# Optimization experiments

Measured on AMD Instinct MI355X. Metric: run time of the kernel, lower is better.

Reference implementation:

```python
import jax, jax.numpy as jnp
import numpy as np

B, T, C = 2, 1024, 2048
H, N = 32, 64
D_DECAY, D_A, D_G = 64, 64, 128
FFN = 8192


def setup_inputs() -> dict:
    key = jax.random.key(0)
    ks = iter(jax.random.split(key, 40))
    def nrm(shape, s):
        return jax.random.normal(next(ks), shape, jnp.float32) * s
    return {
        "x": nrm((B, T, C), 1.0),
        "x_prev": nrm((B, C), 1.0),
        "state": jnp.zeros((B, H, N, N), jnp.float32),
        "ln1_w": jnp.ones((C,), jnp.float32),
        "ln2_w": jnp.ones((C,), jnp.float32),
        "x_r": nrm((C,), 0.1), "x_w": nrm((C,), 0.1), "x_k": nrm((C,), 0.1),
        "x_v": nrm((C,), 0.1), "x_a": nrm((C,), 0.1), "x_g": nrm((C,), 0.1),
        "w0": nrm((C,), 0.1), "w1": nrm((C, D_DECAY), 0.02), "w2": nrm((D_DECAY, C), 0.02),
        "a0": nrm((C,), 0.1), "a1": nrm((C, D_A), 0.02), "a2": nrm((D_A, C), 0.02),
        "g1": nrm((C, D_G), 0.02), "g2": nrm((D_G, C), 0.02),
        "k_k": nrm((C,), 0.1), "k_a": nrm((C,), 0.1), "r_k": nrm((C,), 0.1),
        "R_": nrm((C, C), 0.02), "K_": nrm((C, C), 0.02),
        "V_": nrm((C, C), 0.02), "O_": nrm((C, C), 0.02),
        "gate_w": nrm((FFN, C), 0.02), "up_w": nrm((FFN, C), 0.02),
        "down_w": nrm((C, FFN), 0.02),
    }


def _rmsnorm(h, w, eps=1e-6):
    hf = h.astype(jnp.float32)
    var = jnp.mean(hf * hf, axis=-1, keepdims=True)
    return (w * (hf * jax.lax.rsqrt(var + eps))).astype(h.dtype)


def _lin(x, W):  # nn.Linear weight layout [out, in]
    return jnp.einsum('btc,oc->bto', x, W)


def _rwkv7_scan(r, logw, k, v, a, b, s0):
    # r/logw/k/v/a/b: [B,T,H,N]; s0: [B,H,N,N] (rows=value dim, cols=key dim)
    decay = jnp.exp(logw)  # logw = -exp(w_pre) < 0, per Step2
    def step(S, ins):
        rt, dt, kt, vt, at, bt = ins  # each [B,H,N]
        sa = jnp.einsum('bhvk,bhk->bhv', S, at)
        S = S * dt[:, :, None, :] + sa[..., None] * bt[:, :, None, :] + vt[..., None] * kt[:, :, None, :]
        o = jnp.einsum('bhvk,bhk->bhv', S, rt)
        return S, o
    xs = tuple(jnp.swapaxes(t, 0, 1) for t in (r, decay, k, v, a, b))  # -> [T,B,H,N]
    S, out = jax.lax.scan(step, s0, xs)
    return jnp.swapaxes(out, 0, 1), S  # [B,T,H,N], [B,H,N,N]


def reference(x, x_prev, state, ln1_w, ln2_w, x_r, x_w, x_k, x_v, x_a, x_g,
              w0, w1, w2, a0, a1, a2, g1, g2, k_k, k_a, r_k,
              R_, K_, V_, O_, gate_w, up_w, down_w):
    # ---- ln1 + token shift (Step1), layer_id == 0 so v_first = v ----
    xn = _rmsnorm(x, ln1_w)
    sx = jnp.concatenate([x_prev[:, None, :], xn[:, :-1]], axis=1) - xn
    xr = xn + sx * x_r; xw = xn + sx * x_w; xk = xn + sx * x_k
    xv = xn + sx * x_v; xa = xn + sx * x_a; xg = xn + sx * x_g
    r = _lin(xr, R_)
    w_pre = -jax.nn.softplus(-(w0 + jnp.tanh(xw @ w1) @ w2)) - 0.5
    k = _lin(xk, K_)
    v = _lin(xv, V_)
    a = jax.nn.sigmoid(a0 + (xa @ a1) @ a2)
    g = jax.nn.sigmoid(xg @ g1) @ g2
    kk = (k * k_k).reshape(B, T, H, N)
    kk = kk / jnp.maximum(jnp.linalg.norm(kk, axis=-1, keepdims=True), 1e-12)
    kk = kk.reshape(B, T, C)
    k = k * (1.0 + (a - 1.0) * k_a)
    aa = -kk
    bb = kk * a
    # ---- Step2: RWKV-7 recurrent scan ----
    logw = -jnp.exp(w_pre)
    shp = (B, T, H, N)
    out, new_state = _rwkv7_scan(r.reshape(shp), logw.reshape(shp), k.reshape(shp),
                                 v.reshape(shp), aa.reshape(shp), bb.reshape(shp), state)
    # ---- Step3: bonus term, gate, output proj ----
    xx = out.reshape(B, T, C)
    bonus = ((r * k * r_k).reshape(shp).sum(-1, keepdims=True) * v.reshape(shp)).reshape(B, T, C)
    att = _lin((xx + bonus) * g, O_)
    x = x + att
    # ---- ln2 + SwiGLU MLP ----
    xn2 = _rmsnorm(x, ln2_w)
    mlp = _lin(jax.nn.silu(_lin(xn2, gate_w)) * _lin(xn2, up_w), down_w)
    return x + mlp
```

## Files before the change

kernel.cpp:

```cpp
#include <hip/hip_runtime.h>
#include <hip/hip_bf16.h>
#include <stdint.h>


#define B_   2
#define T_   1024
#define C_   2048
#define H_   32
#define BT_  (B_*T_)
#define FFN_ 8192

typedef unsigned short u16;
typedef __bf16 bf16x8 __attribute__((ext_vector_type(8)));
typedef u16 ushx8 __attribute__((ext_vector_type(8)));
typedef float floatx4 __attribute__((ext_vector_type(4)));

__device__ __forceinline__ float bf2f(u16 v) {
    unsigned int u = ((unsigned int)v) << 16;
    return __builtin_bit_cast(float, u);
}
__device__ __forceinline__ u16 f2bf(float f) {
    unsigned int u = __builtin_bit_cast(unsigned int, f);
    unsigned int lsb = (u >> 16) & 1u;
    u += 0x7fffu + lsb;
    return (u16)(u >> 16);
}

__global__ __launch_bounds__(256) void rmsnorm_kernel(
    const float* __restrict__ in, const float* __restrict__ wgt,
    float* __restrict__ outf, u16* __restrict__ outb, int bf)
{
    int row = blockIdx.x;
    int tid = threadIdx.x;
    const float* xp = in + (size_t)row * C_;
    int c = tid * 8;
    float4 v0 = *(const float4*)&xp[c];
    float4 v1 = *(const float4*)&xp[c + 4];
    float ss = v0.x*v0.x + v0.y*v0.y + v0.z*v0.z + v0.w*v0.w
             + v1.x*v1.x + v1.y*v1.y + v1.z*v1.z + v1.w*v1.w;
    #pragma unroll
    for (int m = 1; m < 64; m <<= 1) ss += __shfl_xor(ss, m, 64);
    __shared__ float red[4];
    if ((tid & 63) == 0) red[tid >> 6] = ss;
    __syncthreads();
    ss = red[0] + red[1] + red[2] + red[3];
    float scale = 1.0f / sqrtf(ss / (float)C_ + 1e-6f);
    float vals[8] = {v0.x, v0.y, v0.z, v0.w, v1.x, v1.y, v1.z, v1.w};
    size_t base = (size_t)row * C_ + c;
    if (bf) {
        #pragma unroll
        for (int j = 0; j < 8; j++) outb[base + j] = f2bf(wgt[c + j] * vals[j] * scale);
    } else {
        #pragma unroll
        for (int j = 0; j < 8; j++) outf[base + j] = wgt[c + j] * vals[j] * scale;
    }
}

__global__ __launch_bounds__(256) void mix_kernel(
    const float* __restrict__ xn, const float* __restrict__ x_prev,
    const float* __restrict__ mr, const float* __restrict__ mw,
    const float* __restrict__ mk, const float* __restrict__ mv,
    const float* __restrict__ ma, const float* __restrict__ mg,
    u16* __restrict__ oxr, u16* __restrict__ oxw, u16* __restrict__ oxk,
    u16* __restrict__ oxv, u16* __restrict__ oxa, u16* __restrict__ oxg)
{
    int row = blockIdx.x;
    int b = row / T_;
    int t = row - b * T_;
    int c = threadIdx.x * 8;
    size_t base = (size_t)row * C_ + c;
    const float* prev = (t == 0) ? (x_prev + (size_t)b * C_ + c) : (xn + base - C_);
    #pragma unroll
    for (int j = 0; j < 8; j++) {
        float xc = xn[base + j];
        float sx = prev[j] - xc;
        int cc = c + j;
        oxr[base + j] = f2bf(xc + sx * mr[cc]);
        oxw[base + j] = f2bf(xc + sx * mw[cc]);
        oxk[base + j] = f2bf(xc + sx * mk[cc]);
        oxv[base + j] = f2bf(xc + sx * mv[cc]);
        oxa[base + j] = f2bf(xc + sx * ma[cc]);
        oxg[base + j] = f2bf(xc + sx * mg[cc]);
    }
}

__global__ __launch_bounds__(256) void cvt_bf16_kernel(
    const float* __restrict__ in, u16* __restrict__ out, long n)
{
    long i = ((long)blockIdx.x * 256 + threadIdx.x) * 4;
    if (i + 3 >= n) return;
    float4 v = *(const float4*)&in[i];
    out[i]     = f2bf(v.x);
    out[i + 1] = f2bf(v.y);
    out[i + 2] = f2bf(v.z);
    out[i + 3] = f2bf(v.w);
}

__global__ __launch_bounds__(256) void transpose_kernel(
    const float* __restrict__ in, u16* __restrict__ out, int rows_in, int cols_in)
{
    long idx = (long)blockIdx.x * 256 + threadIdx.x;
    long total = (long)rows_in * cols_in;
    if (idx >= total) return;
    long o = idx / rows_in;
    long i = idx - o * rows_in;
    out[idx] = f2bf(in[i * (long)cols_in + o]);
}

#define LSTR 40
template<int BN>
__global__ __launch_bounds__(256, 2) void gemm_kernel(
    const u16* __restrict__ A, const u16* __restrict__ W,
    float* __restrict__ Cf, u16* __restrict__ Cb,
    const float* __restrict__ Of, const u16* __restrict__ Ob,
    int M, int N, int K, int mode)
{
    constexpr int IN = BN / 32;
    __shared__ u16 As[128 * LSTR];
    __shared__ u16 Ws[BN * LSTR];
    const int tid = threadIdx.x;
    const int bm = blockIdx.y, bn = blockIdx.x;
    const int row0 = bm * 128, col0 = bn * BN;
    const int wave = tid >> 6, lane = tid & 63;
    const int wr = wave >> 1, wc = wave & 1;
    const int q = lane >> 4, l16 = lane & 15;

    floatx4 acc[4][IN];
    #pragma unroll
    for (int i = 0; i < 4; i++)
        #pragma unroll
        for (int j = 0; j < IN; j++) acc[i][j] = (floatx4){0.f, 0.f, 0.f, 0.f};

    const int r0 = tid >> 2;
    const int cb0 = (tid & 3) * 8;

    for (int k0 = 0; k0 < K; k0 += 32) {
        __syncthreads();
        {
            ushx8 va0 = *(const ushx8*)&A[(size_t)(row0 + r0) * K + k0 + cb0];
            ushx8 vw0 = *(const ushx8*)&W[(size_t)(col0 + r0) * K + k0 + cb0];
            ushx8 va1 = *(const ushx8*)&A[(size_t)(row0 + r0 + 64) * K + k0 + cb0];
            *(ushx8*)&As[r0 * LSTR + cb0] = va0;
            *(ushx8*)&Ws[r0 * LSTR + cb0] = vw0;
            *(ushx8*)&As[(r0 + 64) * LSTR + cb0] = va1;
            if (BN == 128) {
                ushx8 vw1 = *(const ushx8*)&W[(size_t)(col0 + r0 + 64) * K + k0 + cb0];
                *(ushx8*)&Ws[(r0 + 64) * LSTR + cb0] = vw1;
            }
        }
        __syncthreads();
        bf16x8 af[4], wf[IN];
        #pragma unroll
        for (int im = 0; im < 4; im++) {
            int r = wr * 64 + im * 16 + l16;
            af[im] = __builtin_bit_cast(bf16x8, *(const ushx8*)&As[r * LSTR + q * 8]);
        }
        #pragma unroll
        for (int in_ = 0; in_ < IN; in_++) {
            int r = wc * (BN / 2) + in_ * 16 + l16;
            wf[in_] = __builtin_bit_cast(bf16x8, *(const ushx8*)&Ws[r * LSTR + q * 8]);
        }
        #pragma unroll
        for (int im = 0; im < 4; im++)
            #pragma unroll
            for (int in_ = 0; in_ < IN; in_++)
                acc[im][in_] = __builtin_amdgcn_mfma_f32_16x16x32_bf16(
                    af[im], wf[in_], acc[im][in_], 0, 0, 0);
    }

    #pragma unroll
    for (int im = 0; im < 4; im++) {
        #pragma unroll
        for (int in_ = 0; in_ < IN; in_++) {
            #pragma unroll
            for (int rg = 0; rg < 4; rg++) {
                int row = row0 + wr * 64 + im * 16 + q * 4 + rg;
                int col = col0 + wc * (BN / 2) + in_ * 16 + l16;
                if (row < M && col < N) {
                    size_t idx = (size_t)row * N + col;
                    float v = acc[im][in_][rg];
                    switch (mode) {
                        case 0: Cf[idx] = v; break;
                        case 1: Cb[idx] = f2bf(v * bf2f(Ob[idx])); break;
                        case 2: { float s = v / (1.f + expf(-v)); Cb[idx] = f2bf(s); } break;
                        case 3: Cf[idx] = v + Of[idx]; break;
                        case 4: Cb[idx] = f2bf(tanhf(v)); break;
                        case 5: Cb[idx] = f2bf(1.f / (1.f + expf(-v))); break;
                        case 6: Cb[idx] = f2bf(v); break;
                    }
                }
            }
        }
    }
}

__global__ __launch_bounds__(256) void decay_kernel(
    float* __restrict__ z, const float* __restrict__ w0)
{
    long i = (long)blockIdx.x * 256 + threadIdx.x;
    int c = (int)(i & (C_ - 1));
    float zp = w0[c] + z[i];
    float xneg = -zp;
    float sp = (xneg > 20.f) ? xneg : log1pf(expf(xneg));
    float wpre = -sp - 0.5f;
    z[i] = expf(-expf(wpre));
}

__global__ __launch_bounds__(256) void siga_kernel(
    float* __restrict__ z, const float* __restrict__ a0)
{
    long i = (long)blockIdx.x * 256 + threadIdx.x;
    int c = (int)(i & (C_ - 1));
    z[i] = 1.f / (1.f + expf(-(a0[c] + z[i])));
}

__global__ __launch_bounds__(256) void kknorm_kernel(
    float* __restrict__ k, const float* __restrict__ a,
    const float* __restrict__ k_k, const float* __restrict__ k_a,
    float* __restrict__ kk)
{
    int row = blockIdx.x;
    int c = threadIdx.x * 8;
    size_t base = (size_t)row * C_ + c;
    float kl[8], kkl[8];
    float ss = 0.f;
    #pragma unroll
    for (int j = 0; j < 8; j++) {
        kl[j] = k[base + j];
        float t = kl[j] * k_k[c + j];
        kkl[j] = t;
        ss += t * t;
    }
    ss += __shfl_xor(ss, 1, 64);
    ss += __shfl_xor(ss, 2, 64);
    ss += __shfl_xor(ss, 4, 64);
    float inv = 1.f / fmaxf(sqrtf(ss), 1e-12f);
    #pragma unroll
    for (int j = 0; j < 8; j++) {
        kk[base + j] = kkl[j] * inv;
        float av = a[base + j];
        k[base + j] = kl[j] * (1.f + (av - 1.f) * k_a[c + j]);
    }
}

#define SB 16
__global__ __launch_bounds__(256) void scan_kernel(
    const float* __restrict__ rp, const float* __restrict__ dp,
    const float* __restrict__ kp, const float* __restrict__ kkp,
    const float* __restrict__ ap, const float* __restrict__ vp,
    const float* __restrict__ st0, float* __restrict__ xx)
{
    int blk = blockIdx.x;
    int bh = blk >> 2, vblk = blk & 3;
    int b = bh >> 5, h = bh & 31;
    int tid = threadIdx.x;
    int vloc = tid >> 4, kg = tid & 15, c0 = kg * 4;
    int vrow = vblk * 16 + vloc;
    float S0, S1, S2, S3;
    {
        const float* sp = st0 + ((size_t)bh * 64 + vrow) * 64 + c0;
        S0 = sp[0]; S1 = sp[1]; S2 = sp[2]; S3 = sp[3];
    }
    __shared__ float Rs[SB][64], Ds[SB][64], Ks[SB][64], KKs[SB][64], As[SB][64], Vs[SB][64];
    int sidx = (tid * 4) >> 6;
    int nidx = (tid * 4) & 63;
    for (int t0 = 0; t0 < T_; t0 += SB) {
        __syncthreads();
        size_t g = ((size_t)b * T_ + t0 + sidx) * C_ + h * 64 + nidx;
        *(float4*)&Rs[sidx][nidx]  = *(const float4*)&rp[g];
        *(float4*)&Ds[sidx][nidx]  = *(const float4*)&dp[g];
        *(float4*)&Ks[sidx][nidx]  = *(const float4*)&kp[g];
        *(float4*)&KKs[sidx][nidx] = *(const float4*)&kkp[g];
        *(float4*)&As[sidx][nidx]  = *(const float4*)&ap[g];
        *(float4*)&Vs[sidx][nidx]  = *(const float4*)&vp[g];
        __syncthreads();
        for (int s = 0; s < SB; s++) {
            float4 dv  = *(const float4*)&Ds[s][c0];
            float4 kv  = *(const float4*)&Ks[s][c0];
            float4 kkv = *(const float4*)&KKs[s][c0];
            float4 av  = *(const float4*)&As[s][c0];
            float4 rv  = *(const float4*)&Rs[s][c0];
            float vt = Vs[s][vrow];
            float sa = -(S0 * kkv.x + S1 * kkv.y + S2 * kkv.z + S3 * kkv.w);
            sa += __shfl_xor(sa, 1, 64);
            sa += __shfl_xor(sa, 2, 64);
            sa += __shfl_xor(sa, 4, 64);
            sa += __shfl_xor(sa, 8, 64);
            S0 = S0 * dv.x + sa * (kkv.x * av.x) + vt * kv.x;
            S1 = S1 * dv.y + sa * (kkv.y * av.y) + vt * kv.y;
            S2 = S2 * dv.z + sa * (kkv.z * av.z) + vt * kv.z;
            S3 = S3 * dv.w + sa * (kkv.w * av.w) + vt * kv.w;
            float o = S0 * rv.x + S1 * rv.y + S2 * rv.z + S3 * rv.w;
            o += __shfl_xor(o, 1, 64);
            o += __shfl_xor(o, 2, 64);
            o += __shfl_xor(o, 4, 64);
            o += __shfl_xor(o, 8, 64);
            if (kg == 0)
                xx[((size_t)b * T_ + t0 + s) * C_ + h * 64 + vrow] = o;
        }
    }
}

__global__ __launch_bounds__(256) void ygate_kernel(
    const float* __restrict__ xx, const float* __restrict__ r,
    const float* __restrict__ k, const float* __restrict__ r_k,
    const float* __restrict__ v, const float* __restrict__ g,
    u16* __restrict__ y)
{
    int row = blockIdx.x;
    int c = threadIdx.x * 8;
    size_t base = (size_t)row * C_ + c;
    float bsum = 0.f;
    #pragma unroll
    for (int j = 0; j < 8; j++) bsum += r[base + j] * k[base + j] * r_k[c + j];
    bsum += __shfl_xor(bsum, 1, 64);
    bsum += __shfl_xor(bsum, 2, 64);
    bsum += __shfl_xor(bsum, 4, 64);
    #pragma unroll
    for (int j = 0; j < 8; j++) {
        float yv = (xx[base + j] + bsum * v[base + j]) * g[base + j];
        y[base + j] = f2bf(yv);
    }
}

extern "C" void kernel_launch(void* const* d_in, const int* in_sizes, int n_in,
                              void* d_out, int out_size, void* d_ws, size_t ws_size,
                              hipStream_t stream)
{
    const float* x      = (const float*)d_in[0];
    const float* x_prev = (const float*)d_in[1];
    const float* state  = (const float*)d_in[2];
    const float* ln1_w  = (const float*)d_in[3];
    const float* ln2_w  = (const float*)d_in[4];
    const float* x_r = (const float*)d_in[5];
    const float* x_w = (const float*)d_in[6];
    const float* x_k = (const float*)d_in[7];
    const float* x_v = (const float*)d_in[8];
    const float* x_a = (const float*)d_in[9];
    const float* x_g = (const float*)d_in[10];
    const float* w0 = (const float*)d_in[11];
    const float* w1 = (const float*)d_in[12];
    const float* w2 = (const float*)d_in[13];
    const float* a0 = (const float*)d_in[14];
    const float* a1 = (const float*)d_in[15];
    const float* a2 = (const float*)d_in[16];
    const float* g1 = (const float*)d_in[17];
    const float* g2 = (const float*)d_in[18];
    const float* k_k = (const float*)d_in[19];
    const float* k_a = (const float*)d_in[20];
    const float* r_k = (const float*)d_in[21];
    const float* Rw = (const float*)d_in[22];
    const float* Kw = (const float*)d_in[23];
    const float* Vw = (const float*)d_in[24];
    const float* Ow = (const float*)d_in[25];
    const float* gate_w = (const float*)d_in[26];
    const float* up_w   = (const float*)d_in[27];
    const float* down_w = (const float*)d_in[28];
    float* out = (float*)d_out;

    const size_t MBc = 1024ull * 1024ull;
    char* ws = (char*)d_ws;
    u16*  xr_b = (u16*)(ws + 0 * MBc);
    u16*  xw_b = (u16*)(ws + 8 * MBc);
    u16*  xk_b = (u16*)(ws + 16 * MBc);
    u16*  xv_b = (u16*)(ws + 24 * MBc);
    u16*  xa_b = (u16*)(ws + 32 * MBc);
    u16*  xg_b = (u16*)(ws + 40 * MBc);
    float* xn  = (float*)(ws + 48 * MBc);
    float* rb  = (float*)(ws + 48 * MBc);
    float* kb  = (float*)(ws + 64 * MBc);
    float* vb  = (float*)(ws + 80 * MBc);
    float* db  = (float*)(ws + 96 * MBc);
    float* ab  = (float*)(ws + 112 * MBc);
    float* gb  = (float*)(ws + 128 * MBc);
    float* kkb = (float*)(ws + 144 * MBc);
    float* xxb = (float*)(ws + 160 * MBc);
    u16*  yb   = (u16*)(ws + 176 * MBc);
    float* x2  = (float*)(ws + 184 * MBc);
    u16*  xn2b = (u16*)(ws + 200 * MBc);
    u16*  Rb   = (u16*)(ws + 208 * MBc);
    u16*  Kb   = (u16*)(ws + 216 * MBc);
    u16*  Vb   = (u16*)(ws + 224 * MBc);
    u16*  Owb  = (u16*)(ws + 232 * MBc);
    u16*  gateb = (u16*)(ws + 0 * MBc);
    u16*  upb   = (u16*)(ws + 32 * MBc);
    u16*  downb = (u16*)(ws + 64 * MBc);
    u16*  gfb   = (u16*)(ws + 96 * MBc);
    u16*  hb    = (u16*)(ws + 128 * MBc);
    u16*  w2T = (u16*)(ws + 240 * MBc);
    u16*  a2T = (u16*)(ws + 240 * MBc + 256 * 1024);
    u16*  g2T = (u16*)(ws + 240 * MBc + 512 * 1024);
    u16*  t1b = (u16*)(ws + 241 * MBc);
    u16*  t2b = (u16*)(ws + 241 * MBc + 256 * 1024);
    u16*  t3b = (u16*)(ws + 241 * MBc + 512 * 1024);
    u16*  w1T = (u16*)(ws + 160 * MBc);
    u16*  a1T = (u16*)(ws + 160 * MBc + 256 * 1024);
    u16*  g1T = (u16*)(ws + 160 * MBc + 512 * 1024);

    const long cc = (long)C_ * C_;
    const long fc = (long)FFN_ * C_;

    rmsnorm_kernel<<<BT_, 256, 0, stream>>>(x, ln1_w, xn, nullptr, 0);
    mix_kernel<<<BT_, 256, 0, stream>>>(xn, x_prev, x_r, x_w, x_k, x_v, x_a, x_g,
                                        xr_b, xw_b, xk_b, xv_b, xa_b, xg_b);
    cvt_bf16_kernel<<<cc / 1024, 256, 0, stream>>>(Rw, Rb, cc);
    cvt_bf16_kernel<<<cc / 1024, 256, 0, stream>>>(Kw, Kb, cc);
    cvt_bf16_kernel<<<cc / 1024, 256, 0, stream>>>(Vw, Vb, cc);
    cvt_bf16_kernel<<<cc / 1024, 256, 0, stream>>>(Ow, Owb, cc);
    transpose_kernel<<<(64 * C_ + 255) / 256, 256, 0, stream>>>(w2, w2T, 64, C_);
    transpose_kernel<<<(64 * C_ + 255) / 256, 256, 0, stream>>>(a2, a2T, 64, C_);
    transpose_kernel<<<(128 * C_ + 255) / 256, 256, 0, stream>>>(g2, g2T, 128, C_);
    transpose_kernel<<<(64 * C_ + 255) / 256, 256, 0, stream>>>(w1, w1T, C_, 64);
    transpose_kernel<<<(64 * C_ + 255) / 256, 256, 0, stream>>>(a1, a1T, C_, 64);
    transpose_kernel<<<(128 * C_ + 255) / 256, 256, 0, stream>>>(g1, g1T, C_, 128);
    gemm_kernel<128><<<dim3(16, 16), 256, 0, stream>>>(xr_b, Rb, rb, nullptr, nullptr, nullptr, BT_, C_, C_, 0);
    gemm_kernel<128><<<dim3(16, 16), 256, 0, stream>>>(xk_b, Kb, kb, nullptr, nullptr, nullptr, BT_, C_, C_, 0);
    gemm_kernel<128><<<dim3(16, 16), 256, 0, stream>>>(xv_b, Vb, vb, nullptr, nullptr, nullptr, BT_, C_, C_, 0);
    gemm_kernel<64><<<dim3(1, 16), 256, 0, stream>>>(xw_b, w1T, nullptr, t1b, nullptr, nullptr, BT_, 64, C_, 4);
    gemm_kernel<128><<<dim3(16, 16), 256, 0, stream>>>(t1b, w2T, db, nullptr, nullptr, nullptr, BT_, C_, 64, 0);
    decay_kernel<<<(BT_ * C_) / 256, 256, 0, stream>>>(db, w0);
    gemm_kernel<64><<<dim3(1, 16), 256, 0, stream>>>(xa_b, a1T, nullptr, t2b, nullptr, nullptr, BT_, 64, C_, 6);
    gemm_kernel<128><<<dim3(16, 16), 256, 0, stream>>>(t2b, a2T, ab, nullptr, nullptr, nullptr, BT_, C_, 64, 0);
    siga_kernel<<<(BT_ * C_) / 256, 256, 0, stream>>>(ab, a0);
    gemm_kernel<64><<<dim3(2, 16), 256, 0, stream>>>(xg_b, g1T, nullptr, t3b, nullptr, nullptr, BT_, 128, C_, 5);
    gemm_kernel<128><<<dim3(16, 16), 256, 0, stream>>>(t3b, g2T, gb, nullptr, nullptr, nullptr, BT_, C_, 128, 0);
    kknorm_kernel<<<BT_, 256, 0, stream>>>(kb, ab, k_k, k_a, kkb);
    scan_kernel<<<256, 256, 0, stream>>>(rb, db, kb, kkb, ab, vb, state, xxb);
    ygate_kernel<<<BT_, 256, 0, stream>>>(xxb, rb, kb, r_k, vb, gb, yb);
    gemm_kernel<128><<<dim3(16, 16), 256, 0, stream>>>(yb, Owb, x2, nullptr, x, nullptr, BT_, C_, C_, 3);
    cvt_bf16_kernel<<<fc / 1024, 256, 0, stream>>>(gate_w, gateb, fc);
    cvt_bf16_kernel<<<fc / 1024, 256, 0, stream>>>(up_w, upb, fc);
    cvt_bf16_kernel<<<fc / 1024, 256, 0, stream>>>(down_w, downb, fc);
    rmsnorm_kernel<<<BT_, 256, 0, stream>>>(x2, ln2_w, nullptr, xn2b, 1);
    gemm_kernel<128><<<dim3(64, 16), 256, 0, stream>>>(xn2b, gateb, nullptr, gfb, nullptr, nullptr, BT_, FFN_, C_, 2);
    gemm_kernel<128><<<dim3(64, 16), 256, 0, stream>>>(xn2b, upb, nullptr, hb, nullptr, gfb, BT_, FFN_, C_, 1);
    gemm_kernel<128><<<dim3(16, 16), 256, 0, stream>>>(hb, downb, out, nullptr, x2, nullptr, BT_, C_, FFN_, 3);
}
```

Before: 1.604 ms.

## Use direct global-to-LDS loads in GEMM and restructure scan with prefetch and fused reductions

The GEMM now fills its LDS tiles with global_load_lds async copies into an unpadded 32-element stride, replacing the register-staged loads with the padded stride of 40. The scan kernel prefetches the next time block into registers while the current block is computed. It also removes the second shuffle reduction chain by algebraically computing r·S from precomputed per-head k·r and b·r dot products produced in kknorm. The unpadded LDS layout may cause bank conflicts on the fragment reads, and the algebraic rewrite changes floating-point summation order.

```diff
diff --git a/kernel.cpp b/kernel.cpp
--- a/kernel.cpp
+++ b/kernel.cpp
@@ -24,6 +24,12 @@
     unsigned int lsb = (u >> 16) & 1u;
     u += 0x7fffu + lsb;
     return (u16)(u >> 16);
+}
+
+__device__ __forceinline__ void async_copy16(const u16* g, u16* lds) {
+    __builtin_amdgcn_global_load_lds(
+        (const __attribute__((address_space(1))) unsigned int*)g,
+        (__attribute__((address_space(3))) unsigned int*)lds, 16, 0, 0);
 }
 
 __global__ __launch_bounds__(256) void rmsnorm_kernel(
@@ -107,7 +113,6 @@
     out[idx] = f2bf(in[i * (long)cols_in + o]);
 }
 
-#define LSTR 40
 template<int BN>
 __global__ __launch_bounds__(256, 2) void gemm_kernel(
     const u16* __restrict__ A, const u16* __restrict__ W,
@@ -116,49 +121,51 @@
     int M, int N, int K, int mode)
 {
     constexpr int IN = BN / 32;
-    __shared__ u16 As[128 * LSTR];
-    __shared__ u16 Ws[BN * LSTR];
+    __shared__ u16 As[128 * 32];
+    __shared__ u16 Ws[BN * 32];
     const int tid = threadIdx.x;
     const int bm = blockIdx.y, bn = blockIdx.x;
     const int row0 = bm * 128, col0 = bn * BN;
     const int wave = tid >> 6, lane = tid & 63;
     const int wr = wave >> 1, wc = wave & 1;
     const int q = lane >> 4, l16 = lane & 15;
+    const int lr = lane >> 2;
+    const int lc = (lane & 3) * 8;
 
     floatx4 acc[4][IN];
     #pragma unroll
     for (int i = 0; i < 4; i++)
         #pragma unroll
         for (int j = 0; j < IN; j++) acc[i][j] = (floatx4){0.f, 0.f, 0.f, 0.f};
-
-    const int r0 = tid >> 2;
-    const int cb0 = (tid & 3) * 8;
 
     for (int k0 = 0; k0 < K; k0 += 32) {
         __syncthreads();
-        {
-            ushx8 va0 = *(const ushx8*)&A[(size_t)(row0 + r0) * K + k0 + cb0];
-            ushx8 vw0 = *(const ushx8*)&W[(size_t)(col0 + r0) * K + k0 + cb0];
-            ushx8 va1 = *(const ushx8*)&A[(size_t)(row0 + r0 + 64) * K + k0 + cb0];
-            *(ushx8*)&As[r0 * LSTR + cb0] = va0;
-            *(ushx8*)&Ws[r0 * LSTR + cb0] = vw0;
-            *(ushx8*)&As[(r0 + 64) * LSTR + cb0] = va1;
-            if (BN == 128) {
-                ushx8 vw1 = *(const ushx8*)&W[(size_t)(col0 + r0 + 64) * K + k0 + cb0];
-                *(ushx8*)&Ws[(r0 + 64) * LSTR + cb0] = vw1;
+        #pragma unroll
+        for (int j = 0; j < 2; j++) {
+            int r = wave * 32 + j * 16;
+            async_copy16(&A[(size_t)(row0 + r + lr) * K + k0 + lc], &As[r * 32]);
+        }
+        if (BN == 128) {
+            #pragma unroll
+            for (int j = 0; j < 2; j++) {
+                int r = wave * 32 + j * 16;
+                async_copy16(&W[(size_t)(col0 + r + lr) * K + k0 + lc], &Ws[r * 32]);
             }
+        } else {
+            int r = wave * 16;
+            async_copy16(&W[(size_t)(col0 + r + lr) * K + k0 + lc], &Ws[r * 32]);
         }
         __syncthreads();
         bf16x8 af[4], wf[IN];
         #pragma unroll
         for (int im = 0; im < 4; im++) {
             int r = wr * 64 + im * 16 + l16;
-            af[im] = __builtin_bit_cast(bf16x8, *(const ushx8*)&As[r * LSTR + q * 8]);
+            af[im] = __builtin_bit_cast(bf16x8, *(const ushx8*)&As[r * 32 + q * 8]);
         }
         #pragma unroll
         for (int in_ = 0; in_ < IN; in_++) {
             int r = wc * (BN / 2) + in_ * 16 + l16;
-            wf[in_] = __builtin_bit_cast(bf16x8, *(const ushx8*)&Ws[r * LSTR + q * 8]);
+            wf[in_] = __builtin_bit_cast(bf16x8, *(const ushx8*)&Ws[r * 32 + q * 8]);
         }
         #pragma unroll
         for (int im = 0; im < 4; im++)
@@ -217,16 +224,20 @@
 __global__ __launch_bounds__(256) void kknorm_kernel(
     float* __restrict__ k, const float* __restrict__ a,
     const float* __restrict__ k_k, const float* __restrict__ k_a,
-    float* __restrict__ kk)
+    const float* __restrict__ r, float* __restrict__ kk,
+    float* __restrict__ kr, float* __restrict__ br)
 {
     int row = blockIdx.x;
-    int c = threadIdx.x * 8;
+    int tid = threadIdx.x;
+    int c = tid * 8;
+    int h = tid >> 3, j8 = tid & 7;
     size_t base = (size_t)row * C_ + c;
-    float kl[8], kkl[8];
+    float kl[8], kkl[8], al[8];
     float ss = 0.f;
     #pragma unroll
     for (int j = 0; j < 8; j++) {
         kl[j] = k[base + j];
+        al[j] = a[base + j];
         float t = kl[j] * k_k[c + j];
         kkl[j] = t;
         ss += t * t;
@@ -235,11 +246,23 @@
     ss += __shfl_xor(ss, 2, 64);
     ss += __shfl_xor(ss, 4, 64);
     float inv = 1.f / fmaxf(sqrtf(ss), 1e-12f);
+    float krp = 0.f, brp = 0.f;
     #pragma unroll
     for (int j = 0; j < 8; j++) {
-        kk[base + j] = kkl[j] * inv;
-        float av = a[base + j];
-        k[base + j] = kl[j] * (1.f + (av - 1.f) * k_a[c + j]);
+        float kkv = kkl[j] * inv;
+        kk[base + j] = kkv;
+        float knew = kl[j] * (1.f + (al[j] - 1.f) * k_a[c + j]);
+        k[base + j] = knew;
+        float rv = r[base + j];
+        krp += knew * rv;
+        brp += kkv * al[j] * rv;
+    }
+    krp += __shfl_xor(krp, 1, 64); brp += __shfl_xor(brp, 1, 64);
+    krp += __shfl_xor(krp, 2, 64); brp += __shfl_xor(brp, 2, 64);
+    krp += __shfl_xor(krp, 4, 64); brp += __shfl_xor(brp, 4, 64);
+    if (j8 == 0) {
+        kr[(size_t)row * H_ + h] = krp;
+        br[(size_t)row * H_ + h] = brp;
     }
 }
 
@@ -248,6 +271,7 @@
     const float* __restrict__ rp, const float* __restrict__ dp,
     const float* __restrict__ kp, const float* __restrict__ kkp,
     const float* __restrict__ ap, const float* __restrict__ vp,
+    const float* __restrict__ krp, const float* __restrict__ brp,
     const float* __restrict__ st0, float* __restrict__ xx)
 {
     int blk = blockIdx.x;
@@ -262,18 +286,50 @@
         S0 = sp[0]; S1 = sp[1]; S2 = sp[2]; S3 = sp[3];
     }
     __shared__ float Rs[SB][64], Ds[SB][64], Ks[SB][64], KKs[SB][64], As[SB][64], Vs[SB][64];
+    __shared__ float KRs[SB], BRs[SB];
     int sidx = (tid * 4) >> 6;
     int nidx = (tid * 4) & 63;
+    size_t gstep = (size_t)(b * T_) * C_ + h * 64 + nidx;
+
+    float4 pr, pd, pk, pkk, pa, pv;
+    float pkr = 0.f, pbr = 0.f;
+    {
+        size_t g = gstep + (size_t)sidx * C_;
+        pr  = *(const float4*)&rp[g];
+        pd  = *(const float4*)&dp[g];
+        pk  = *(const float4*)&kp[g];
+        pkk = *(const float4*)&kkp[g];
+        pa  = *(const float4*)&ap[g];
+        pv  = *(const float4*)&vp[g];
+        if (tid < SB) {
+            pkr = krp[(size_t)(b * T_ + tid) * H_ + h];
+            pbr = brp[(size_t)(b * T_ + tid) * H_ + h];
+        }
+    }
+
     for (int t0 = 0; t0 < T_; t0 += SB) {
+        *(float4*)&Rs[sidx][nidx]  = pr;
+        *(float4*)&Ds[sidx][nidx]  = pd;
+        *(float4*)&Ks[sidx][nidx]  = pk;
+        *(float4*)&KKs[sidx][nidx] = pkk;
+        *(float4*)&As[sidx][nidx]  = pa;
+        *(float4*)&Vs[sidx][nidx]  = pv;
+        if (tid < SB) { KRs[tid] = pkr; BRs[tid] = pbr; }
         __syncthreads();
-        size_t g = ((size_t)b * T_ + t0 + sidx) * C_ + h * 64 + nidx;
-        *(float4*)&Rs[sidx][nidx]  = *(const float4*)&rp[g];
-        *(float4*)&Ds[sidx][nidx]  = *(const float4*)&dp[g];
-        *(float4*)&Ks[sidx][nidx]  = *(const float4*)&kp[g];
-        *(float4*)&KKs[sidx][nidx] = *(const float4*)&kkp[g];
-        *(float4*)&As[sidx][nidx]  = *(const float4*)&ap[g];
-        *(float4*)&Vs[sidx][nidx]  = *(const float4*)&vp[g];
-        __syncthreads();
+        if (t0 + SB < T_) {
+            size_t g = gstep + (size_t)(t0 + SB + sidx) * C_;
+            pr  = *(const float4*)&rp[g];
+            pd  = *(const float4*)&dp[g];
+            pk  = *(const float4*)&kp[g];
+            pkk = *(const float4*)&kkp[g];
+            pa  = *(const float4*)&ap[g];
+            pv  = *(const float4*)&vp[g];
+            if (tid < SB) {
+                pkr = krp[(size_t)(b * T_ + t0 + SB + tid) * H_ + h];
+                pbr = brp[(size_t)(b * T_ + t0 + SB + tid) * H_ + h];
+            }
+        }
+        #pragma unroll 4
         for (int s = 0; s < SB; s++) {
             float4 dv  = *(const float4*)&Ds[s][c0];
             float4 kv  = *(const float4*)&Ks[s][c0];
@@ -281,23 +337,30 @@
             float4 av  = *(const float4*)&As[s][c0];
             float4 rv  = *(const float4*)&Rs[s][c0];
             float vt = Vs[s][vrow];
-            float sa = -(S0 * kkv.x + S1 * kkv.y + S2 * kkv.z + S3 * kkv.w);
-            sa += __shfl_xor(sa, 1, 64);
-            sa += __shfl_xor(sa, 2, 64);
-            sa += __shfl_xor(sa, 4, 64);
-            sa += __shfl_xor(sa, 8, 64);
-            S0 = S0 * dv.x + sa * (kkv.x * av.x) + vt * kv.x;
-            S1 = S1 * dv.y + sa * (kkv.y * av.y) + vt * kv.y;
-            S2 = S2 * dv.z + sa * (kkv.z * av.z) + vt * kv.z;
-            S3 = S3 * dv.w + sa * (kkv.w * av.w) + vt * kv.w;
-            float o = S0 * rv.x + S1 * rv.y + S2 * rv.z + S3 * rv.w;
-            o += __shfl_xor(o, 1, 64);
-            o += __shfl_xor(o, 2, 64);
-            o += __shfl_xor(o, 4, 64);
-            o += __shfl_xor(o, 8, 64);
-            if (kg == 0)
+            float krt = KRs[s], brt = BRs[s];
+            float sa = -((S0 * kkv.x + S1 * kkv.y) + (S2 * kkv.z + S3 * kkv.w));
+            float rd = (S0 * (dv.x * rv.x) + S1 * (dv.y * rv.y))
+                     + (S2 * (dv.z * rv.z) + S3 * (dv.w * rv.w));
+            float bx = kkv.x * av.x, by = kkv.y * av.y, bz = kkv.z * av.z, bw = kkv.w * av.w;
+            float base0 = fmaf(S0, dv.x, vt * kv.x);
+            float base1 = fmaf(S1, dv.y, vt * kv.y);
+            float base2 = fmaf(S2, dv.z, vt * kv.z);
+            float base3 = fmaf(S3, dv.w, vt * kv.w);
+            sa += __shfl_xor(sa, 1, 64); rd += __shfl_xor(rd, 1, 64);
+            sa += __shfl_xor(sa, 2, 64); rd += __shfl_xor(rd, 2, 64);
+            sa += __shfl_xor(sa, 4, 64); rd += __shfl_xor(rd, 4, 64);
+            sa += __shfl_xor(sa, 8, 64); rd += __shfl_xor(rd, 8, 64);
+            S0 = fmaf(sa, bx, base0);
+            S1 = fmaf(sa, by, base1);
+            S2 = fmaf(sa, bz, base2);
+            S3 = fmaf(sa, bw, base3);
+            if (kg == 0) {
+                float o = fmaf(sa, brt, rd);
+                o = fmaf(vt, krt, o);
                 xx[((size_t)b * T_ + t0 + s) * C_ + h * 64 + vrow] = o;
-        }
+            }
+        }
+        __syncthreads();
     }
 }
 
@@ -396,6 +459,8 @@
     u16*  w1T = (u16*)(ws + 160 * MBc);
     u16*  a1T = (u16*)(ws + 160 * MBc + 256 * 1024);
     u16*  g1T = (u16*)(ws + 160 * MBc + 512 * 1024);
+    float* krb = (float*)(ws + 176 * MBc);
+    float* brb = (float*)(ws + 176 * MBc + 256 * 1024);
 
     const long cc = (long)C_ * C_;
     const long fc = (long)FFN_ * C_;
@@ -424,8 +489,8 @@
     siga_kernel<<<(BT_ * C_) / 256, 256, 0, stream>>>(ab, a0);
     gemm_kernel<64><<<dim3(2, 16), 256, 0, stream>>>(xg_b, g1T, nullptr, t3b, nullptr, nullptr, BT_, 128, C_, 5);
     gemm_kernel<128><<<dim3(16, 16), 256, 0, stream>>>(t3b, g2T, gb, nullptr, nullptr, nullptr, BT_, C_, 128, 0);
-    kknorm_kernel<<<BT_, 256, 0, stream>>>(kb, ab, k_k, k_a, kkb);
-    scan_kernel<<<256, 256, 0, stream>>>(rb, db, kb, kkb, ab, vb, state, xxb);
+    kknorm_kernel<<<BT_, 256, 0, stream>>>(kb, ab, k_k, k_a, rb, kkb, krb, brb);
+    scan_kernel<<<256, 256, 0, stream>>>(rb, db, kb, kkb, ab, vb, krb, brb, state, xxb);
     ygate_kernel<<<BT_, 256, 0, stream>>>(xxb, rb, kb, r_k, vb, gb, yb);
     gemm_kernel<128><<<dim3(16, 16), 256, 0, stream>>>(yb, Owb, x2, nullptr, x, nullptr, BT_, C_, C_, 3);
     cvt_bf16_kernel<<<fc / 1024, 256, 0, stream>>>(gate_w, gateb, fc);
```

Result: faster. 1.500 ms (-6.5%).
